# Performance work log

Measured on AMD Instinct MI355X. Metric: run time of the kernel, lower is better.

Reference implementation:

```python
import jax, jax.numpy as jnp
import numpy as np

DIM = 512
NUM_HEADS = 8
HEAD_DIM = DIM // NUM_HEADS
MAX_SIZE = 128


def setup_inputs() -> dict:
    key = jax.random.key(0)
    ks = jax.random.split(key, 13)
    B, C, H, W = 4, DIM, 128, 128
    inp = {
        "x": jax.random.normal(ks[0], (B, C, H, W), jnp.float32),
        "q_w": jax.random.normal(ks[1], (DIM, DIM), jnp.float32) * 0.02,
        "q_b": jax.random.normal(ks[2], (DIM,), jnp.float32) * 0.02,
        "k_w": jax.random.normal(ks[3], (DIM, DIM), jnp.float32) * 0.02,
        "k_b": jax.random.normal(ks[4], (DIM,), jnp.float32) * 0.02,
        "v_w": jax.random.normal(ks[5], (DIM, DIM), jnp.float32) * 0.02,
        "v_b": jax.random.normal(ks[6], (DIM,), jnp.float32) * 0.02,
        "o_w": jax.random.normal(ks[7], (DIM, DIM), jnp.float32) * 0.02,
        "o_b": jax.random.normal(ks[8], (DIM,), jnp.float32) * 0.02,
        "pos_q": jax.random.normal(ks[9], (1, NUM_HEADS, MAX_SIZE, HEAD_DIM), jnp.float32),
        "pos_k": jax.random.normal(ks[10], (1, NUM_HEADS, MAX_SIZE, HEAD_DIM), jnp.float32),
        "pos_v": jax.random.normal(ks[11], (1, NUM_HEADS, MAX_SIZE, HEAD_DIM), jnp.float32),
        "g_q": jnp.ones((1,), jnp.float32),
        "g_k": jnp.ones((1,), jnp.float32),
        "g_v1": jnp.ones((1,), jnp.float32),
        "g_v2": jnp.ones((1,), jnp.float32),
    }
    return inp


def _gated_axial_attn(x, q_w, q_b, k_w, k_b, v_w, v_b, o_w, o_b,
                      pos_q, pos_k, pos_v, g_q, g_k, g_v1, g_v2):
    B, C, H, W = x.shape
    nh, hd = NUM_HEADS, C // NUM_HEADS
    scale = hd ** (-0.5)
    # axis='width': attend along W for each (B,H) row
    xf = jnp.transpose(x, (0, 2, 3, 1)).reshape(B * H, W, C)  # (BH, W, C)

    def proj(w, b):
        y = xf @ w.T + b                       # (BH, W, C)
        return jnp.transpose(y.reshape(B * H, W, nh, hd), (0, 2, 1, 3))  # (BH, nh, W, hd)

    q = proj(q_w, q_b)
    k = proj(k_w, k_b)
    v = proj(v_w, v_b)

    pq = pos_q[0, :, :W, :]  # (nh, W, hd)
    pk = pos_k[0, :, :W, :]
    pv = pos_v[0, :, :W, :]

    # scores[i,j] = q_i.k_j + g_q * q_i.pq_j + g_k * pk_i.k_j, all scaled
    scores = jnp.einsum('bnid,bnjd->bnij', q, k)
    scores = scores + g_q[0] * jnp.einsum('bnid,njd->bnij', q, pq)
    scores = scores + g_k[0] * jnp.einsum('nid,bnjd->bnij', pk, k)
    attn = jax.nn.softmax(scores * scale, axis=-1)  # (BH, nh, W, W)

    vmix = g_v1[0] * v + g_v2[0] * pv[None]        # (BH, nh, W, hd)
    out = jnp.einsum('bnij,bnjd->bnid', attn, vmix)
    out = jnp.transpose(out, (0, 2, 1, 3)).reshape(B * H, W, C)
    out = out @ o_w.T + o_b
    return jnp.transpose(out.reshape(B, H, W, C), (0, 3, 1, 2))  # (B, C, H, W)


def reference(x, q_w, q_b, k_w, k_b, v_w, v_b, o_w, o_b,
              pos_q, pos_k, pos_v, g_q, g_k, g_v1, g_v2):
    return _gated_axial_attn(x, q_w, q_b, k_w, k_b, v_w, v_b, o_w, o_b,
                             pos_q, pos_k, pos_v, g_q, g_k, g_v1, g_v2)
```

## Files before the change

kernel.cpp:

```cpp
#include <hip/hip_runtime.h>

typedef __bf16 bf16;
typedef __attribute__((ext_vector_type(8))) __bf16 bf16x8;
typedef __attribute__((ext_vector_type(4))) __bf16 bf16x4;
typedef __attribute__((ext_vector_type(4))) float fvec4;

#define MFMA16(a, b, c) __builtin_amdgcn_mfma_f32_16x16x32_bf16(a, b, c, 0, 0, 0)

__device__ __forceinline__ void glds16(const bf16* g, bf16* l) {
  __builtin_amdgcn_global_load_lds(
      (const __attribute__((address_space(1))) void*)g,
      (__attribute__((address_space(3))) void*)l, 16, 0, 0);
}

__device__ inline fvec4 zero4() { fvec4 z = {0.f, 0.f, 0.f, 0.f}; return z; }

#define PREP_ELEMS 1245184

__global__ __launch_bounds__(512) void prep_kernel(
    const float* __restrict__ qw, const float* __restrict__ kw,
    const float* __restrict__ vw, const float* __restrict__ ow,
    const float* __restrict__ pq, const float* __restrict__ pk,
    const float* __restrict__ pv, bf16* __restrict__ dst)
{
  int i = (blockIdx.x * 512 + threadIdx.x) * 4;
  const float* s;
  if      (i < 262144)  s = qw + i;
  else if (i < 524288)  s = kw + (i - 262144);
  else if (i < 786432)  s = vw + (i - 524288);
  else if (i < 1048576) s = ow + (i - 786432);
  else if (i < 1114112) s = pq + (i - 1048576);
  else if (i < 1179648) s = pk + (i - 1114112);
  else                  s = pv + (i - 1179648);
  fvec4 v = *(const fvec4*)s;
  bf16x4 o = { (bf16)v[0], (bf16)v[1], (bf16)v[2], (bf16)v[3] };
  *(bf16x4*)(dst + i) = o;
}

__global__ __launch_bounds__(256) void xpose_kernel(
    const float* __restrict__ x, bf16* __restrict__ xt, int bh0)
{
  __shared__ float Xs[64 * 133];
  const int cb = blockIdx.x, lb = blockIdx.y;
  const int bh = bh0 + lb, b = bh >> 7, h = bh & 127;
  const int t = threadIdx.x;
  const float* xb = x + (size_t)b * 8388608 + (size_t)(cb * 64) * 16384 + h * 128;
  #pragma unroll
  for (int it = 0; it < 8; ++it) {
    int idx = it * 256 + t;
    int c = idx >> 5, w4 = (idx & 31) << 2;
    fvec4 v = *(const fvec4*)(xb + (size_t)c * 16384 + w4);
    #pragma unroll
    for (int j = 0; j < 4; ++j) Xs[c * 133 + w4 + j] = v[j];
  }
  __syncthreads();
  const int c0 = (t & 7) * 8, wsub = t >> 3;
  #pragma unroll
  for (int wb = 0; wb < 4; ++wb) {
    int w = wb * 32 + wsub;
    bf16x8 o;
    #pragma unroll
    for (int i = 0; i < 8; ++i) o[i] = (bf16)Xs[(c0 + i) * 133 + w];
    *(bf16x8*)(xt + ((size_t)lb * 128 + w) * 512 + cb * 64 + c0) = o;
  }
}

__global__ __launch_bounds__(256, 3) void qkvgemm_kernel(
    const bf16* __restrict__ xt, const bf16* __restrict__ wqkv,
    const float* __restrict__ q_b, const float* __restrict__ k_b,
    const float* __restrict__ v_b, bf16* __restrict__ qkvbuf)
{
  __shared__ bf16 As[128 * 64];
  __shared__ bf16 Bs[128 * 64];
  const int nt0 = blockIdx.x * 128;
  const int m0 = blockIdx.y * 128;
  const int t = threadIdx.x;
  const int wv = t >> 6, lane = t & 63;
  const int lr = lane & 15, lg = lane >> 4;
  const int wm = wv >> 1, wn = wv & 1;
  const int srow = lane >> 3, c16 = lane & 7;

  fvec4 acc[4][4];
  #pragma unroll
  for (int i = 0; i < 4; ++i)
    #pragma unroll
    for (int j = 0; j < 4; ++j) acc[i][j] = zero4();

  for (int k0 = 0; k0 < 512; k0 += 64) {
    __syncthreads();
    #pragma unroll
    for (int j = 0; j < 4; ++j) {
      int seg = wv * 4 + j;
      int row = seg * 8 + srow;
      int cs = c16 ^ (row & 7);
      glds16(xt + (size_t)(m0 + row) * 512 + k0 + cs * 8, As + seg * 512);
      glds16(wqkv + (size_t)(nt0 + row) * 512 + k0 + cs * 8, Bs + seg * 512);
    }
    __syncthreads();
    #pragma unroll
    for (int kc = 0; kc < 2; ++kc) {
      bf16x8 af[4], bfv[4];
      #pragma unroll
      for (int mt = 0; mt < 4; ++mt) {
        int row = wm * 64 + mt * 16 + lr;
        int cs = (kc * 4 + lg) ^ (row & 7);
        af[mt] = *(const bf16x8*)(As + row * 64 + cs * 8);
      }
      #pragma unroll
      for (int nt = 0; nt < 4; ++nt) {
        int row = wn * 64 + nt * 16 + lr;
        int cs = (kc * 4 + lg) ^ (row & 7);
        bfv[nt] = *(const bf16x8*)(Bs + row * 64 + cs * 8);
      }
      #pragma unroll
      for (int mt = 0; mt < 4; ++mt)
        #pragma unroll
        for (int nt = 0; nt < 4; ++nt)
          acc[mt][nt] = MFMA16(af[mt], bfv[nt], acc[mt][nt]);
    }
  }
  #pragma unroll
  for (int nt = 0; nt < 4; ++nt) {
    int col = nt0 + wn * 64 + nt * 16 + lr;
    int cr = col & 511;
    const float* bias = (col < 512) ? q_b : ((col < 1024) ? k_b : v_b);
    float bv = bias[cr];
    #pragma unroll
    for (int mt = 0; mt < 4; ++mt) {
      int mb = m0 + wm * 64 + mt * 16 + lg * 4;
      #pragma unroll
      for (int r = 0; r < 4; ++r)
        qkvbuf[(size_t)(mb + r) * 1536 + col] = (bf16)(acc[mt][nt][r] + bv);
    }
  }
}

__global__ __launch_bounds__(512, 2) void attn_kernel(
    const bf16* __restrict__ qkvbuf, const bf16* __restrict__ posb,
    const float* __restrict__ g_q, const float* __restrict__ g_k,
    const float* __restrict__ g_v1, const float* __restrict__ g_v2,
    bf16* __restrict__ ao)
{
  __shared__ bf16 KP[128 * 136];
  __shared__ bf16 Vt[64 * 136];
  const int blk = blockIdx.x;
  const int lb = blk >> 3, n = blk & 7;
  const float gq = g_q[0], gk = g_k[0];
  const float gv1 = g_v1[0], gv2 = g_v2[0];
  const bf16* Qb = qkvbuf + (size_t)(lb * 128) * 1536 + n * 64;
  const bf16* Kb = Qb + 512;
  const bf16* Vb = Qb + 1024;
  const bf16* pqb = posb + (size_t)n * 8192;
  const bf16* pkb = posb + 65536 + (size_t)n * 8192;
  const bf16* pvb = posb + 131072 + (size_t)n * 8192;
  const int t = threadIdx.x;

  #pragma unroll
  for (int it = 0; it < 2; ++it) {
    int idx = it * 512 + t;
    int j = idx >> 3, d0 = (idx & 7) << 3;
    bf16x8 kv  = *(const bf16x8*)(Kb + (size_t)j * 1536 + d0);
    bf16x8 pq8 = *(const bf16x8*)(pqb + j * 64 + d0);
    bf16x8 r1;
    #pragma unroll
    for (int i = 0; i < 8; ++i) r1[i] = (bf16)((float)kv[i] + gq * (float)pq8[i]);
    *(bf16x8*)(&KP[j * 136 + d0]) = r1;
    *(bf16x8*)(&KP[j * 136 + 64 + d0]) = kv;
    bf16x8 vv  = *(const bf16x8*)(Vb + (size_t)j * 1536 + d0);
    bf16x8 pv8 = *(const bf16x8*)(pvb + j * 64 + d0);
    #pragma unroll
    for (int i = 0; i < 8; ++i)
      Vt[(d0 + i) * 136 + j] = (bf16)(gv1 * (float)vv[i] + gv2 * (float)pv8[i]);
  }
  __syncthreads();

  const int wv = t >> 6, l = t & 63, lr = l & 15, lg = l >> 4;
  const int i0 = wv * 16;

  fvec4 s[8];
  #pragma unroll
  for (int i = 0; i < 8; ++i) s[i] = zero4();
  for (int kc = 0; kc < 4; ++kc) {
    bf16x8 af;
    if (kc < 2) {
      af = *(const bf16x8*)(Qb + (size_t)(i0 + lr) * 1536 + kc * 32 + lg * 8);
    } else {
      bf16x8 raw = *(const bf16x8*)(pkb + (i0 + lr) * 64 + (kc - 2) * 32 + lg * 8);
      #pragma unroll
      for (int i = 0; i < 8; ++i) af[i] = (bf16)(gk * (float)raw[i]);
    }
    #pragma unroll
    for (int jt = 0; jt < 8; ++jt) {
      bf16x8 bfr = *(const bf16x8*)(&KP[(jt * 16 + lr) * 136 + kc * 32 + lg * 8]);
      s[jt] = MFMA16(af, bfr, s[jt]);
    }
  }

  const float scale = 0.125f;
  float inv[4];
  #pragma unroll
  for (int r = 0; r < 4; ++r) {
    float m = -1e30f;
    #pragma unroll
    for (int jt = 0; jt < 8; ++jt) m = fmaxf(m, s[jt][r]);
    #pragma unroll
    for (int off = 1; off < 16; off <<= 1) m = fmaxf(m, __shfl_xor(m, off));
    float sm = 0.f;
    #pragma unroll
    for (int jt = 0; jt < 8; ++jt) {
      float e = __expf((s[jt][r] - m) * scale);
      s[jt][r] = e;
      sm += e;
    }
    #pragma unroll
    for (int off = 1; off < 16; off <<= 1) sm += __shfl_xor(sm, off);
    inv[r] = 1.f / sm;
  }
  __syncthreads();
  #pragma unroll
  for (int r = 0; r < 4; ++r) {
    int i = i0 + lg * 4 + r;
    #pragma unroll
    for (int jt = 0; jt < 8; ++jt)
      KP[i * 136 + jt * 16 + lr] = (bf16)(s[jt][r] * inv[r]);
  }
  __syncthreads();

  fvec4 o[4];
  #pragma unroll
  for (int i = 0; i < 4; ++i) o[i] = zero4();
  for (int kc = 0; kc < 4; ++kc) {
    bf16x8 af = *(const bf16x8*)(&KP[(i0 + lr) * 136 + kc * 32 + lg * 8]);
    #pragma unroll
    for (int dt = 0; dt < 4; ++dt) {
      bf16x8 bfr = *(const bf16x8*)(&Vt[(dt * 16 + lr) * 136 + kc * 32 + lg * 8]);
      o[dt] = MFMA16(af, bfr, o[dt]);
    }
  }
  #pragma unroll
  for (int dt = 0; dt < 4; ++dt) {
    #pragma unroll
    for (int r = 0; r < 4; ++r) {
      int i = i0 + lg * 4 + r;
      ao[((size_t)lb * 128 + i) * 512 + n * 64 + dt * 16 + lr] = (bf16)o[dt][r];
    }
  }
}

__global__ __launch_bounds__(256, 3) void oproj_kernel(
    const bf16* __restrict__ ao, const bf16* __restrict__ wo,
    const float* __restrict__ o_b, float* __restrict__ out, int bh0)
{
  __shared__ bf16 As[128 * 64];
  __shared__ bf16 Bs[128 * 64];
  const int ct4 = blockIdx.x;
  const int lb = blockIdx.y;
  const int bh = bh0 + lb, b = bh >> 7, h = bh & 127;
  const int t = threadIdx.x;
  const int wv = t >> 6, lane = t & 63;
  const int lr = lane & 15, lg = lane >> 4;
  const int wm = wv >> 1, wn = wv & 1;
  const int srow = lane >> 3, c16 = lane & 7;

  fvec4 acc[4][4];
  #pragma unroll
  for (int i = 0; i < 4; ++i)
    #pragma unroll
    for (int j = 0; j < 4; ++j) acc[i][j] = zero4();

  for (int k0 = 0; k0 < 512; k0 += 64) {
    __syncthreads();
    #pragma unroll
    for (int j = 0; j < 4; ++j) {
      int seg = wv * 4 + j;
      int row = seg * 8 + srow;
      int cs = c16 ^ (row & 7);
      glds16(wo + (size_t)(ct4 * 128 + row) * 512 + k0 + cs * 8, As + seg * 512);
      glds16(ao + ((size_t)lb * 128 + row) * 512 + k0 + cs * 8, Bs + seg * 512);
    }
    __syncthreads();
    #pragma unroll
    for (int kc = 0; kc < 2; ++kc) {
      bf16x8 af[4], bfv[4];
      #pragma unroll
      for (int mt = 0; mt < 4; ++mt) {
        int row = wm * 64 + mt * 16 + lr;
        int cs = (kc * 4 + lg) ^ (row & 7);
        af[mt] = *(const bf16x8*)(As + row * 64 + cs * 8);
      }
      #pragma unroll
      for (int nt = 0; nt < 4; ++nt) {
        int row = wn * 64 + nt * 16 + lr;
        int cs = (kc * 4 + lg) ^ (row & 7);
        bfv[nt] = *(const bf16x8*)(Bs + row * 64 + cs * 8);
      }
      #pragma unroll
      for (int mt = 0; mt < 4; ++mt)
        #pragma unroll
        for (int nt = 0; nt < 4; ++nt)
          acc[mt][nt] = MFMA16(af[mt], bfv[nt], acc[mt][nt]);
    }
  }
  #pragma unroll
  for (int mt = 0; mt < 4; ++mt) {
    #pragma unroll
    for (int r = 0; r < 4; ++r) {
      int co = ct4 * 128 + wm * 64 + mt * 16 + lg * 4 + r;
      float bv = o_b[co];
      size_t ob = ((size_t)(b * 512 + co) * 128 + h) * 128;
      #pragma unroll
      for (int nt = 0; nt < 4; ++nt) {
        int w = wn * 64 + nt * 16 + lr;
        out[ob + w] = acc[mt][nt][r] + bv;
      }
    }
  }
}

extern "C" void kernel_launch(void* const* d_in, const int* in_sizes, int n_in,
                              void* d_out, int out_size, void* d_ws, size_t ws_size,
                              hipStream_t stream) {
  const float* x    = (const float*)d_in[0];
  const float* q_w  = (const float*)d_in[1];
  const float* q_b  = (const float*)d_in[2];
  const float* k_w  = (const float*)d_in[3];
  const float* k_b  = (const float*)d_in[4];
  const float* v_w  = (const float*)d_in[5];
  const float* v_b  = (const float*)d_in[6];
  const float* o_w  = (const float*)d_in[7];
  const float* o_b  = (const float*)d_in[8];
  const float* pos_q = (const float*)d_in[9];
  const float* pos_k = (const float*)d_in[10];
  const float* pos_v = (const float*)d_in[11];
  const float* g_q  = (const float*)d_in[12];
  const float* g_k  = (const float*)d_in[13];
  const float* g_v1 = (const float*)d_in[14];
  const float* g_v2 = (const float*)d_in[15];
  float* out = (float*)d_out;

  bf16* prep = (bf16*)d_ws;
  bf16* wqkv = prep;
  bf16* wo   = prep + 786432;
  bf16* posb = prep + 1048576;

  bf16* rest = prep + PREP_ELEMS;
  size_t avail = (ws_size > (size_t)PREP_ELEMS * 2) ? ws_size - (size_t)PREP_ELEMS * 2 : 0;
  const size_t per_bh = (size_t)(65536 + 196608) * sizeof(bf16);
  int nbh = (int)(avail / per_bh);
  if (nbh > 512) nbh = 512;
  if (nbh < 1) nbh = 1;

  bf16* xt = rest;
  bf16* qkvbuf = xt + (size_t)nbh * 65536;

  prep_kernel<<<608, 512, 0, stream>>>(q_w, k_w, v_w, o_w, pos_q, pos_k, pos_v, prep);

  for (int bh0 = 0; bh0 < 512; bh0 += nbh) {
    int cur = (512 - bh0 < nbh) ? (512 - bh0) : nbh;
    xpose_kernel<<<dim3(8, cur), 256, 0, stream>>>(x, xt, bh0);
    qkvgemm_kernel<<<dim3(12, cur), 256, 0, stream>>>(xt, wqkv, q_b, k_b, v_b, qkvbuf);
    attn_kernel<<<cur * 8, 512, 0, stream>>>(qkvbuf, posb, g_q, g_k, g_v1, g_v2, xt);
    oproj_kernel<<<dim3(4, cur), 256, 0, stream>>>(xt, wo, o_b, out, bh0);
  }
}
```

Measured before the change: 531.9 us.

## Remap GEMM workgroups XCD-aware and cap chunk size for L2 residency

```diff
diff --git a/kernel.cpp b/kernel.cpp
--- a/kernel.cpp
+++ b/kernel.cpp
@@ -72,8 +72,12 @@
 {
   __shared__ bf16 As[128 * 64];
   __shared__ bf16 Bs[128 * 64];
-  const int nt0 = blockIdx.x * 128;
-  const int m0 = blockIdx.y * 128;
+  const int nwg = gridDim.x;
+  int wg = blockIdx.x;
+  if ((nwg & 7) == 0) wg = (wg & 7) * (nwg >> 3) + (wg >> 3);
+  const int mt = wg / 12;
+  const int nt0 = (wg - mt * 12) * 128;
+  const int m0 = mt * 128;
   const int t = threadIdx.x;
   const int wv = t >> 6, lane = t & 63;
   const int lr = lane & 15, lg = lane >> 4;
@@ -101,10 +105,10 @@
     for (int kc = 0; kc < 2; ++kc) {
       bf16x8 af[4], bfv[4];
       #pragma unroll
-      for (int mt = 0; mt < 4; ++mt) {
-        int row = wm * 64 + mt * 16 + lr;
+      for (int mt2 = 0; mt2 < 4; ++mt2) {
+        int row = wm * 64 + mt2 * 16 + lr;
         int cs = (kc * 4 + lg) ^ (row & 7);
-        af[mt] = *(const bf16x8*)(As + row * 64 + cs * 8);
+        af[mt2] = *(const bf16x8*)(As + row * 64 + cs * 8);
       }
       #pragma unroll
       for (int nt = 0; nt < 4; ++nt) {
@@ -113,10 +117,10 @@
         bfv[nt] = *(const bf16x8*)(Bs + row * 64 + cs * 8);
       }
       #pragma unroll
-      for (int mt = 0; mt < 4; ++mt)
+      for (int mt2 = 0; mt2 < 4; ++mt2)
         #pragma unroll
         for (int nt = 0; nt < 4; ++nt)
-          acc[mt][nt] = MFMA16(af[mt], bfv[nt], acc[mt][nt]);
+          acc[mt2][nt] = MFMA16(af[mt2], bfv[nt], acc[mt2][nt]);
     }
   }
   #pragma unroll
@@ -126,11 +130,11 @@
     const float* bias = (col < 512) ? q_b : ((col < 1024) ? k_b : v_b);
     float bv = bias[cr];
     #pragma unroll
-    for (int mt = 0; mt < 4; ++mt) {
-      int mb = m0 + wm * 64 + mt * 16 + lg * 4;
+    for (int mt2 = 0; mt2 < 4; ++mt2) {
+      int mb = m0 + wm * 64 + mt2 * 16 + lg * 4;
       #pragma unroll
       for (int r = 0; r < 4; ++r)
-        qkvbuf[(size_t)(mb + r) * 1536 + col] = (bf16)(acc[mt][nt][r] + bv);
+        qkvbuf[(size_t)(mb + r) * 1536 + col] = (bf16)(acc[mt2][nt][r] + bv);
     }
   }
 }
@@ -253,8 +257,11 @@
 {
   __shared__ bf16 As[128 * 64];
   __shared__ bf16 Bs[128 * 64];
-  const int ct4 = blockIdx.x;
-  const int lb = blockIdx.y;
+  const int nwg = gridDim.x;
+  int wg = blockIdx.x;
+  if ((nwg & 7) == 0) wg = (wg & 7) * (nwg >> 3) + (wg >> 3);
+  const int ct4 = wg & 3;
+  const int lb = wg >> 2;
   const int bh = bh0 + lb, b = bh >> 7, h = bh & 127;
   const int t = threadIdx.x;
   const int wv = t >> 6, lane = t & 63;
@@ -347,7 +354,7 @@
   size_t avail = (ws_size > (size_t)PREP_ELEMS * 2) ? ws_size - (size_t)PREP_ELEMS * 2 : 0;
   const size_t per_bh = (size_t)(65536 + 196608) * sizeof(bf16);
   int nbh = (int)(avail / per_bh);
-  if (nbh > 512) nbh = 512;
+  if (nbh > 128) nbh = 128;
   if (nbh < 1) nbh = 1;
 
   bf16* xt = rest;
@@ -358,8 +365,8 @@
   for (int bh0 = 0; bh0 < 512; bh0 += nbh) {
     int cur = (512 - bh0 < nbh) ? (512 - bh0) : nbh;
     xpose_kernel<<<dim3(8, cur), 256, 0, stream>>>(x, xt, bh0);
-    qkvgemm_kernel<<<dim3(12, cur), 256, 0, stream>>>(xt, wqkv, q_b, k_b, v_b, qkvbuf);
+    qkvgemm_kernel<<<cur * 12, 256, 0, stream>>>(xt, wqkv, q_b, k_b, v_b, qkvbuf);
     attn_kernel<<<cur * 8, 512, 0, stream>>>(qkvbuf, posb, g_q, g_k, g_v1, g_v2, xt);
-    oproj_kernel<<<dim3(4, cur), 256, 0, stream>>>(xt, wo, o_b, out, bh0);
-  }
-}
+    oproj_kernel<<<cur * 4, 256, 0, stream>>>(xt, wo, o_b, out, bh0);
+  }
+}
```

New measurement: 510.5 us. 4.0% less time.
